# Kernel optimization log

Hardware: AMD Instinct MI355X
Metric: run time of the kernel (lower is better)

Reference implementation:

```python
import jax, jax.numpy as jnp
import numpy as np

B, S, P, D, H = 2, 2048, 2048, 2048, 16
HD = D // H  # head_dim = 128


def setup_inputs() -> dict:
    key = jax.random.key(0)
    ks = jax.random.split(key, 8)
    scale = 1.0 / np.sqrt(D)
    return {
        "x": jax.random.normal(ks[0], (B, S, D), jnp.float32),
        "cache_k": jax.random.normal(ks[1], (B, P, D), jnp.float32),
        "cache_v": jax.random.normal(ks[2], (B, P, D), jnp.float32),
        "wq": jax.random.normal(ks[3], (D, D), jnp.float32) * scale,
        "bq": jnp.zeros((D,), jnp.float32),
        "wk": jax.random.normal(ks[4], (D, D), jnp.float32) * scale,
        "bk": jnp.zeros((D,), jnp.float32),
        "wv": jax.random.normal(ks[5], (D, D), jnp.float32) * scale,
        "bv": jnp.zeros((D,), jnp.float32),
        "wo": jax.random.normal(ks[6], (D, D), jnp.float32) * scale,
        "bo": jnp.zeros((D,), jnp.float32),
    }


def reference(x, cache_k, cache_v, wq, bq, wk, bk, wv, bv, wo, bo):
    bsz, seq_len, _ = x.shape
    q = x @ wq + bq                      # [B,S,D]
    k_new = x @ wk + bk                  # [B,S,D]
    v_new = x @ wv + bv
    # use_cache=True path: prepend cached (detached) keys/values
    k = jnp.concatenate([cache_k, k_new], axis=1)  # [B,P+S,D]
    v = jnp.concatenate([cache_v, v_new], axis=1)
    # split heads: [B,H,S,hd] / [B,H,K,hd]
    q = q.reshape(bsz, seq_len, H, HD).transpose(0, 2, 1, 3)
    k = k.reshape(bsz, -1, H, HD).transpose(0, 2, 1, 3)
    v = v.reshape(bsz, -1, H, HD).transpose(0, 2, 1, 3)
    scores = jnp.einsum("bhsd,bhkd->bhsk", q, k) / jnp.sqrt(jnp.float32(HD))
    attn = jax.nn.softmax(scores, axis=-1)          # full-softmax, no mask
    out = jnp.einsum("bhsk,bhkd->bhsd", attn, v)
    out = out.transpose(0, 2, 1, 3).reshape(bsz, seq_len, D)
    return out @ wo + bo
```

## Files before the change

kernel.cpp:

```cpp
#include <hip/hip_runtime.h>

typedef __attribute__((ext_vector_type(8))) short short8;
typedef __attribute__((ext_vector_type(4))) short short4_;
typedef __attribute__((ext_vector_type(4))) float f32x4;

#define AS1 __attribute__((address_space(1)))
#define AS3 __attribute__((address_space(3)))
#define GLD16(g, l) __builtin_amdgcn_global_load_lds((const AS1 void*)(g), (AS3 void*)(l), 16, 0, 0)

#define C2 0.12751743f

__device__ __forceinline__ unsigned short f2bf(float f) {
  unsigned int u = __float_as_uint(f);
  u += 0x7fffu + ((u >> 16) & 1u);
  return (unsigned short)(u >> 16);
}

__global__ __launch_bounds__(256) void k_transpose_w(
    const float* __restrict__ wq, const float* __restrict__ wk,
    const float* __restrict__ wv, const float* __restrict__ wo,
    unsigned short* __restrict__ wqkvT, unsigned short* __restrict__ woT)
{
  __shared__ float tile[64][65];
  const int z = blockIdx.z;
  const float* src = (z == 0) ? wq : (z == 1) ? wk : (z == 2) ? wv : wo;
  unsigned short* dst = (z == 3) ? woT : (wqkvT + (size_t)z * 2048 * 2048);
  const int k0 = blockIdx.y * 64, n0 = blockIdx.x * 64;
  const int tid = threadIdx.x;
#pragma unroll
  for (int p = 0; p < 4; ++p) {
    const int r = p * 16 + (tid >> 4);
    const int c = (tid & 15) * 4;
    f32x4 v = *(const f32x4*)(src + (size_t)(k0 + r) * 2048 + n0 + c);
    tile[r][c + 0] = v[0]; tile[r][c + 1] = v[1];
    tile[r][c + 2] = v[2]; tile[r][c + 3] = v[3];
  }
  __syncthreads();
#pragma unroll
  for (int p = 0; p < 2; ++p) {
    const int task = tid + p * 256;
    const int n = task >> 3;
    const int kc = (task & 7) * 8;
    short8 ov;
#pragma unroll
    for (int j = 0; j < 8; ++j) ov[j] = (short)f2bf(tile[kc + j][n]);
    *(short8*)(dst + (size_t)(n0 + n) * 2048 + k0 + kc) = ov;
  }
}

__global__ __launch_bounds__(256) void k_convert(
    const float* __restrict__ x, const float* __restrict__ ck, const float* __restrict__ cv,
    unsigned short* __restrict__ xbf, unsigned short* __restrict__ kfull,
    unsigned short* __restrict__ vfull)
{
  const int z = blockIdx.y;
  const size_t idx = ((size_t)blockIdx.x * 256 + threadIdx.x) * 8;
  const float* src = (z == 0) ? x : (z == 1) ? ck : cv;
  f32x4 a = *(const f32x4*)(src + idx);
  f32x4 b = *(const f32x4*)(src + idx + 4);
  short8 ov;
#pragma unroll
  for (int j = 0; j < 4; ++j) { ov[j] = (short)f2bf(a[j]); ov[j + 4] = (short)f2bf(b[j]); }
  unsigned short* dp; size_t di;
  if (z == 0) { dp = xbf; di = idx; }
  else {
    const size_t r = idx >> 11, cl = idx & 2047;
    const size_t orow = r + (r & ~(size_t)2047);
    di = orow * 2048 + cl;
    dp = (z == 1) ? kfull : vfull;
  }
  *(short8*)(dp + di) = ov;
}

template <int MODE>
__global__ __launch_bounds__(256, 2) void k_gemm(
    const unsigned short* __restrict__ A, const unsigned short* __restrict__ BT,
    unsigned short* __restrict__ Oq, unsigned short* __restrict__ Ok,
    unsigned short* __restrict__ Ov, float* __restrict__ Of,
    const float* __restrict__ b0, const float* __restrict__ b1,
    const float* __restrict__ b2, int K)
{
  __shared__ unsigned short Ah[128 * 32];
  __shared__ unsigned short Bh[128 * 32];
  const int tid = threadIdx.x;
  const int l = tid & 63, w = tid >> 6;
  const int l15 = l & 15, g = l >> 4;
  const int wr = (w >> 1) * 64, wc = (w & 1) * 64;
  const int bm = blockIdx.y, bn = blockIdx.x;
  const unsigned short* Ab = A + (size_t)bm * 128 * K;
  const unsigned short* Bb = BT + (size_t)bn * 128 * K;
  const int srow = l >> 2;
  const int scol = (l & 3) * 8;
  f32x4 acc[4][4];
#pragma unroll
  for (int i = 0; i < 4; ++i)
#pragma unroll
    for (int j = 0; j < 4; ++j)
#pragma unroll
      for (int e = 0; e < 4; ++e) acc[i][j][e] = 0.f;

  for (int kt = 0; kt < K; kt += 32) {
#pragma unroll
    for (int cc = 0; cc < 2; ++cc) {
      const int c = w + cc * 4;
      GLD16(Ab + (size_t)(c * 16 + srow) * K + kt + scol, &Ah[c * 512]);
      GLD16(Bb + (size_t)(c * 16 + srow) * K + kt + scol, &Bh[c * 512]);
    }
    __syncthreads();
    short8 af[4], bf[4];
#pragma unroll
    for (int i = 0; i < 4; ++i) {
      af[i] = *(const short8*)&Ah[(wr + i * 16 + l15) * 32 + g * 8];
      bf[i] = *(const short8*)&Bh[(wc + i * 16 + l15) * 32 + g * 8];
    }
#pragma unroll
    for (int i = 0; i < 4; ++i)
#pragma unroll
      for (int j = 0; j < 4; ++j)
        acc[i][j] = __builtin_amdgcn_mfma_f32_16x16x32_bf16(af[i], bf[j], acc[i][j], 0, 0, 0);
    __syncthreads();
  }

  const int rbase = bm * 128 + wr + g * 4;
  if (MODE == 0) {
    const int nglob = bn * 128;
    const int which = nglob >> 11;
    const int ncol0 = nglob & 2047;
    unsigned short* dst = (which == 0) ? Oq : (which == 1) ? Ok : Ov;
    const float* bias = (which == 0) ? b0 : (which == 1) ? b1 : b2;
#pragma unroll
    for (int j = 0; j < 4; ++j) {
      const int cc = ncol0 + wc + j * 16 + l15;
      const float bb = bias[cc];
#pragma unroll
      for (int i = 0; i < 4; ++i) {
#pragma unroll
        for (int ii = 0; ii < 4; ++ii) {
          const int rr = rbase + i * 16 + ii;
          const size_t orow = (which == 0) ? (size_t)rr
                                           : (size_t)(rr + (rr & ~2047) + 2048);
          dst[orow * 2048 + cc] = f2bf(acc[i][j][ii] + bb);
        }
      }
    }
  } else {
#pragma unroll
    for (int j = 0; j < 4; ++j) {
      const int cc = bn * 128 + wc + j * 16 + l15;
      const float bb = b0[cc];
#pragma unroll
      for (int i = 0; i < 4; ++i) {
#pragma unroll
        for (int ii = 0; ii < 4; ++ii) {
          const int rr = rbase + i * 16 + ii;
          Of[(size_t)rr * 2048 + cc] = acc[i][j][ii] + bb;
        }
      }
    }
  }
}

__global__ __launch_bounds__(256, 2) void k_flash(
    const unsigned short* __restrict__ qbuf, const unsigned short* __restrict__ kfull,
    const unsigned short* __restrict__ vfull, unsigned short* __restrict__ attnout)
{
  __shared__ char smem[65536];
  unsigned short* Kl = (unsigned short*)smem;
  unsigned short* Vt = (unsigned short*)(smem + 32768);
  const int tid = threadIdx.x;
  const int l = tid & 63, w = tid >> 6;
  const int l15 = l & 15, g = l >> 4, l7 = l & 7;
  const int qt = blockIdx.x, bh = blockIdx.y;
  const int b = bh >> 4, h = bh & 15;

  short8 qf[4];
  {
    const int qrow = qt * 64 + w * 16 + l15;
    const unsigned short* qp = qbuf + ((size_t)(b * 2048 + qrow)) * 2048 + h * 128 + g * 8;
    qf[0] = *(const short8*)(qp);
    qf[1] = *(const short8*)(qp + 32);
    qf[2] = *(const short8*)(qp + 64);
    qf[3] = *(const short8*)(qp + 96);
  }
  f32x4 o[8];
#pragma unroll
  for (int d = 0; d < 8; ++d)
#pragma unroll
    for (int e = 0; e < 4; ++e) o[d][e] = 0.f;
  float m = -3.0e38f, lsum = 0.f;

  const int srowK = l >> 4;
  const int suK = l & 15;

  for (int t = 0; t < 32; ++t) {
    const size_t kt0 = (size_t)t * 128;
    const unsigned short* kb = kfull + ((size_t)b * 4096 + kt0) * 2048 + h * 128;
    const unsigned short* vb = vfull + ((size_t)b * 4096 + kt0) * 2048 + h * 128;
#pragma unroll
    for (int ci = 0; ci < 8; ++ci) {
      const int c = w * 8 + ci;
      const int row = c * 4 + srowK;
      const int ucol = (suK ^ (row & 7)) * 8;
      GLD16(kb + (size_t)row * 2048 + ucol, &Kl[c * 512]);
    }
#pragma unroll
    for (int p = 0; p < 2; ++p) {
      const int task = tid + p * 256;
      const int g4 = task & 31;
      const int dc = task >> 5;
      const unsigned short* vp = vb + (size_t)(g4 * 4) * 2048 + dc * 8;
      short8 r0 = *(const short8*)(vp);
      short8 r1 = *(const short8*)(vp + 2048);
      short8 r2 = *(const short8*)(vp + 4096);
      short8 r3 = *(const short8*)(vp + 6144);
      const int vcol4 = (g4 & ~7) | ((g4 & 3) << 1) | ((g4 >> 2) & 1);
#pragma unroll
      for (int d = 0; d < 8; ++d) {
        const int row = dc * 8 + d;
        short4_ pk; pk[0] = r0[d]; pk[1] = r1[d]; pk[2] = r2[d]; pk[3] = r3[d];
        const int unit16 = (vcol4 >> 1) ^ (row & 7);
        *(short4_*)((char*)Vt + row * 256 + unit16 * 16 + (vcol4 & 1) * 8) = pk;
      }
    }
    __syncthreads();
    f32x4 sc[8];
#pragma unroll
    for (int kc = 0; kc < 8; ++kc) {
      f32x4 a4;
#pragma unroll
      for (int e = 0; e < 4; ++e) a4[e] = 0.f;
      const int row = kc * 16 + l15;
#pragma unroll
      for (int kk = 0; kk < 4; ++kk) {
        const int unit = (kk * 4 + g) ^ (row & 7);
        short8 af = *(const short8*)((const char*)Kl + row * 256 + unit * 16);
        a4 = __builtin_amdgcn_mfma_f32_16x16x32_bf16(af, qf[kk], a4, 0, 0, 0);
      }
      sc[kc] = a4;
    }
    float tm = -3.0e38f;
#pragma unroll
    for (int kc = 0; kc < 8; ++kc)
#pragma unroll
      for (int i = 0; i < 4; ++i) tm = fmaxf(tm, sc[kc][i]);
    tm = fmaxf(tm, __shfl_xor(tm, 16, 64));
    tm = fmaxf(tm, __shfl_xor(tm, 32, 64));
    const float mnew = fmaxf(m, tm);
    const float f = exp2f(C2 * (m - mnew));
    m = mnew;
    float psum = 0.f;
    short8 pf[4];
#pragma unroll
    for (int c = 0; c < 4; ++c) {
#pragma unroll
      for (int i = 0; i < 4; ++i) {
        const float p0 = exp2f(C2 * (sc[2 * c][i] - mnew));
        const float p1 = exp2f(C2 * (sc[2 * c + 1][i] - mnew));
        psum += p0 + p1;
        pf[c][i] = (short)f2bf(p0);
        pf[c][i + 4] = (short)f2bf(p1);
      }
    }
    psum += __shfl_xor(psum, 16, 64);
    psum += __shfl_xor(psum, 32, 64);
    lsum = lsum * f + psum;
#pragma unroll
    for (int d = 0; d < 8; ++d)
#pragma unroll
      for (int e = 0; e < 4; ++e) o[d][e] *= f;
#pragma unroll
    for (int c = 0; c < 4; ++c) {
#pragma unroll
      for (int d = 0; d < 8; ++d) {
        const int row = d * 16 + l15;
        const int unit = (4 * c + g) ^ l7;
        short8 vf = *(const short8*)((const char*)Vt + row * 256 + unit * 16);
        o[d] = __builtin_amdgcn_mfma_f32_16x16x32_bf16(vf, pf[c], o[d], 0, 0, 0);
      }
    }
    __syncthreads();
  }
  const float inv = 1.0f / lsum;
  float* ep = (float*)smem;
#pragma unroll
  for (int d = 0; d < 8; ++d) {
    f32x4 tv;
#pragma unroll
    for (int e = 0; e < 4; ++e) tv[e] = o[d][e] * inv;
    *(f32x4*)(ep + (w * 16 + l15) * 132 + d * 16 + g * 4) = tv;
  }
  __syncthreads();
#pragma unroll
  for (int p = 0; p < 4; ++p) {
    const int task = tid + p * 256;
    const int row = task >> 4, ch = task & 15;
    const float* sp = ep + row * 132 + ch * 8;
    short8 ov;
#pragma unroll
    for (int j = 0; j < 8; ++j) ov[j] = (short)f2bf(sp[j]);
    const int qg = qt * 64 + row;
    *(short8*)(attnout + ((size_t)(b * 2048 + qg)) * 2048 + h * 128 + ch * 8) = ov;
  }
}

extern "C" void kernel_launch(void* const* d_in, const int* in_sizes, int n_in,
                              void* d_out, int out_size, void* d_ws, size_t ws_size,
                              hipStream_t stream)
{
  const float* x  = (const float*)d_in[0];
  const float* ck = (const float*)d_in[1];
  const float* cv = (const float*)d_in[2];
  const float* wq = (const float*)d_in[3];
  const float* bq = (const float*)d_in[4];
  const float* wk = (const float*)d_in[5];
  const float* bk = (const float*)d_in[6];
  const float* wv = (const float*)d_in[7];
  const float* bv = (const float*)d_in[8];
  const float* wo = (const float*)d_in[9];
  const float* bo = (const float*)d_in[10];
  float* out = (float*)d_out;

  char* ws = (char*)d_ws;
  unsigned short* xbf   = (unsigned short*)(ws);
  unsigned short* wqkvT = (unsigned short*)(ws + 16777216ull);
  unsigned short* woT   = (unsigned short*)(ws + 41943040ull);
  unsigned short* qbuf  = (unsigned short*)(ws + 50331648ull);
  unsigned short* kfull = (unsigned short*)(ws + 67108864ull);
  unsigned short* vfull = (unsigned short*)(ws + 100663296ull);
  unsigned short* aout  = (unsigned short*)(ws + 134217728ull);

  k_transpose_w<<<dim3(32, 32, 4), 256, 0, stream>>>(wq, wk, wv, wo, wqkvT, woT);
  k_convert<<<dim3(4096, 3), 256, 0, stream>>>(x, ck, cv, xbf, kfull, vfull);
  k_gemm<0><<<dim3(48, 32), 256, 0, stream>>>(xbf, wqkvT, qbuf, kfull, vfull, nullptr,
                                              bq, bk, bv, 2048);
  k_flash<<<dim3(32, 32), 256, 0, stream>>>(qbuf, kfull, vfull, aout);
  k_gemm<1><<<dim3(16, 32), 256, 0, stream>>>(aout, woT, nullptr, nullptr, nullptr, out,
                                              bo, nullptr, nullptr, 2048);
}
```

Before: 682.8 us.

## Double-buffer K/V tiles, process two query tiles per wave, lazy rescale

Rewrites the flash-attention kernel so each block handles 128 query rows (two 16-row sets per wave) and reuses every K/V fragment loaded from LDS for both sets. K/V tiles shrink to 64 keys and are double-buffered, so the next tile is prefetched while the current one is computed, and priority hints are added around the MFMA sections. The running-max rescale is skipped unless the max grows by more than a threshold, and the epilogue now goes through bf16 staging. Risks are higher register pressure with two accumulator sets, and half as many blocks in the grid.

```diff
diff --git a/kernel.cpp b/kernel.cpp
--- a/kernel.cpp
+++ b/kernel.cpp
@@ -165,141 +165,212 @@
     const unsigned short* __restrict__ vfull, unsigned short* __restrict__ attnout)
 {
   __shared__ char smem[65536];
-  unsigned short* Kl = (unsigned short*)smem;
-  unsigned short* Vt = (unsigned short*)(smem + 32768);
   const int tid = threadIdx.x;
   const int l = tid & 63, w = tid >> 6;
-  const int l15 = l & 15, g = l >> 4, l7 = l & 7;
+  const int l15 = l & 15, g = l >> 4;
   const int qt = blockIdx.x, bh = blockIdx.y;
   const int b = bh >> 4, h = bh & 15;
 
-  short8 qf[4];
+  short8 qfA[4], qfB[4];
   {
-    const int qrow = qt * 64 + w * 16 + l15;
-    const unsigned short* qp = qbuf + ((size_t)(b * 2048 + qrow)) * 2048 + h * 128 + g * 8;
-    qf[0] = *(const short8*)(qp);
-    qf[1] = *(const short8*)(qp + 32);
-    qf[2] = *(const short8*)(qp + 64);
-    qf[3] = *(const short8*)(qp + 96);
-  }
-  f32x4 o[8];
+    const int qrowA = qt * 128 + w * 32 + l15;
+    const unsigned short* qpA = qbuf + ((size_t)(b * 2048 + qrowA)) * 2048 + h * 128 + g * 8;
+    const unsigned short* qpB = qpA + 16 * 2048;
+#pragma unroll
+    for (int kk = 0; kk < 4; ++kk) {
+      qfA[kk] = *(const short8*)(qpA + kk * 32);
+      qfB[kk] = *(const short8*)(qpB + kk * 32);
+    }
+  }
+  f32x4 oA[8], oB[8];
 #pragma unroll
   for (int d = 0; d < 8; ++d)
 #pragma unroll
-    for (int e = 0; e < 4; ++e) o[d][e] = 0.f;
-  float m = -3.0e38f, lsum = 0.f;
-
-  const int srowK = l >> 4;
-  const int suK = l & 15;
-
-  for (int t = 0; t < 32; ++t) {
-    const size_t kt0 = (size_t)t * 128;
-    const unsigned short* kb = kfull + ((size_t)b * 4096 + kt0) * 2048 + h * 128;
-    const unsigned short* vb = vfull + ((size_t)b * 4096 + kt0) * 2048 + h * 128;
-#pragma unroll
-    for (int ci = 0; ci < 8; ++ci) {
-      const int c = w * 8 + ci;
-      const int row = c * 4 + srowK;
-      const int ucol = (suK ^ (row & 7)) * 8;
-      GLD16(kb + (size_t)row * 2048 + ucol, &Kl[c * 512]);
-    }
-#pragma unroll
-    for (int p = 0; p < 2; ++p) {
-      const int task = tid + p * 256;
-      const int g4 = task & 31;
-      const int dc = task >> 5;
-      const unsigned short* vp = vb + (size_t)(g4 * 4) * 2048 + dc * 8;
-      short8 r0 = *(const short8*)(vp);
-      short8 r1 = *(const short8*)(vp + 2048);
-      short8 r2 = *(const short8*)(vp + 4096);
-      short8 r3 = *(const short8*)(vp + 6144);
-      const int vcol4 = (g4 & ~7) | ((g4 & 3) << 1) | ((g4 >> 2) & 1);
+    for (int e = 0; e < 4; ++e) { oA[d][e] = 0.f; oB[d][e] = 0.f; }
+  float mA = -1e30f, mB = -1e30f, lsA = 0.f, lsB = 0.f;
+
+  const unsigned short* kbase = kfull + ((size_t)b * 4096) * 2048 + h * 128;
+  const unsigned short* vbase = vfull + ((size_t)b * 4096) * 2048 + h * 128;
+
+  const int vg4 = tid & 15;
+  const int vdc = tid >> 4;
+  const int vcol4 = (vg4 & 8) | ((vg4 & 3) << 1) | ((vg4 >> 2) & 1);
+  const int vu = vcol4 >> 1;
+  const int vhalf = (vcol4 & 1) * 8;
+  const int ksrow = l >> 4, ksu = l & 15;
+
+  auto STAGEK = [&](int t, char* Kn) {
+    const unsigned short* kb = kbase + (size_t)t * 64 * 2048;
+#pragma unroll
+    for (int ci = 0; ci < 4; ++ci) {
+      const int c = w * 4 + ci;
+      const int row = c * 4 + ksrow;
+      GLD16(kb + (size_t)row * 2048 + ((ksu ^ (row & 7)) * 8), Kn + c * 1024);
+    }
+  };
+  auto VLOAD = [&](int t, short8* r) {
+    const unsigned short* vp = vbase + ((size_t)t * 64 + vg4 * 4) * 2048 + vdc * 8;
+    r[0] = *(const short8*)(vp);
+    r[1] = *(const short8*)(vp + 2048);
+    r[2] = *(const short8*)(vp + 4096);
+    r[3] = *(const short8*)(vp + 6144);
+  };
+  auto VWRITE = [&](char* Vn, short8* r) {
+#pragma unroll
+    for (int d = 0; d < 8; ++d) {
+      const int row = vdc * 8 + d;
+      const int mm = (d ^ vdc) & 7;
+      short4_ pk; pk[0] = r[0][d]; pk[1] = r[1][d]; pk[2] = r[2][d]; pk[3] = r[3][d];
+      *(short4_*)(Vn + row * 128 + ((vu ^ mm) * 16) + vhalf) = pk;
+    }
+  };
+
+  {
+    short8 vr[4];
+    STAGEK(0, smem);
+    VLOAD(0, vr);
+    VWRITE(smem + 16384, vr);
+    __syncthreads();
+  }
+
+  for (int t = 0; t < 64; ++t) {
+    char* Kc = smem + (t & 1) * 32768;
+    char* Vc = Kc + 16384;
+    char* Kn = smem + ((t + 1) & 1) * 32768;
+    char* Vn = Kn + 16384;
+    const bool pre = (t + 1) < 64;
+    short8 vr[4];
+    if (pre) {
+      STAGEK(t + 1, Kn);
+      VLOAD(t + 1, vr);
+    }
+    f32x4 scA[4], scB[4];
+    __builtin_amdgcn_s_setprio(1);
+#pragma unroll
+    for (int kc = 0; kc < 4; ++kc) {
+      f32x4 a0, a1;
+#pragma unroll
+      for (int e = 0; e < 4; ++e) { a0[e] = 0.f; a1[e] = 0.f; }
+      const int rowk = kc * 16 + l15;
+      const int mk = rowk & 7;
+#pragma unroll
+      for (int kk = 0; kk < 4; ++kk) {
+        short8 kf = *(const short8*)(Kc + rowk * 256 + (((kk * 4 + g) ^ mk) * 16));
+        a0 = __builtin_amdgcn_mfma_f32_16x16x32_bf16(kf, qfA[kk], a0, 0, 0, 0);
+        a1 = __builtin_amdgcn_mfma_f32_16x16x32_bf16(kf, qfB[kk], a1, 0, 0, 0);
+      }
+      scA[kc] = a0; scB[kc] = a1;
+    }
+    __builtin_amdgcn_s_setprio(0);
+    if (pre) VWRITE(Vn, vr);
+
+    short8 pfA[2], pfB[2];
+    {
+      float tm = fmaxf(fmaxf(scA[0][0], scA[0][1]), fmaxf(scA[0][2], scA[0][3]));
+#pragma unroll
+      for (int kc = 1; kc < 4; ++kc)
+        tm = fmaxf(tm, fmaxf(fmaxf(scA[kc][0], scA[kc][1]), fmaxf(scA[kc][2], scA[kc][3])));
+      tm = fmaxf(tm, __shfl_xor(tm, 16, 64));
+      tm = fmaxf(tm, __shfl_xor(tm, 32, 64));
+      if (!__all(tm <= mA + 16.f)) {
+        const float mn = fmaxf(mA, tm);
+        const float f = exp2f(C2 * (mA - mn));
+        mA = mn; lsA *= f;
+#pragma unroll
+        for (int d = 0; d < 8; ++d)
+#pragma unroll
+          for (int e = 0; e < 4; ++e) oA[d][e] *= f;
+      }
+      const float mc = C2 * mA;
+      float ps = 0.f;
+#pragma unroll
+      for (int c = 0; c < 2; ++c) {
+#pragma unroll
+        for (int i = 0; i < 4; ++i) {
+          const float p0 = exp2f(fmaf(C2, scA[2 * c][i], -mc));
+          const float p1 = exp2f(fmaf(C2, scA[2 * c + 1][i], -mc));
+          ps += p0 + p1;
+          pfA[c][i] = (short)f2bf(p0);
+          pfA[c][i + 4] = (short)f2bf(p1);
+        }
+      }
+      ps += __shfl_xor(ps, 16, 64);
+      ps += __shfl_xor(ps, 32, 64);
+      lsA += ps;
+    }
+    {
+      float tm = fmaxf(fmaxf(scB[0][0], scB[0][1]), fmaxf(scB[0][2], scB[0][3]));
+#pragma unroll
+      for (int kc = 1; kc < 4; ++kc)
+        tm = fmaxf(tm, fmaxf(fmaxf(scB[kc][0], scB[kc][1]), fmaxf(scB[kc][2], scB[kc][3])));
+      tm = fmaxf(tm, __shfl_xor(tm, 16, 64));
+      tm = fmaxf(tm, __shfl_xor(tm, 32, 64));
+      if (!__all(tm <= mB + 16.f)) {
+        const float mn = fmaxf(mB, tm);
+        const float f = exp2f(C2 * (mB - mn));
+        mB = mn; lsB *= f;
+#pragma unroll
+        for (int d = 0; d < 8; ++d)
+#pragma unroll
+          for (int e = 0; e < 4; ++e) oB[d][e] *= f;
+      }
+      const float mc = C2 * mB;
+      float ps = 0.f;
+#pragma unroll
+      for (int c = 0; c < 2; ++c) {
+#pragma unroll
+        for (int i = 0; i < 4; ++i) {
+          const float p0 = exp2f(fmaf(C2, scB[2 * c][i], -mc));
+          const float p1 = exp2f(fmaf(C2, scB[2 * c + 1][i], -mc));
+          ps += p0 + p1;
+          pfB[c][i] = (short)f2bf(p0);
+          pfB[c][i + 4] = (short)f2bf(p1);
+        }
+      }
+      ps += __shfl_xor(ps, 16, 64);
+      ps += __shfl_xor(ps, 32, 64);
+      lsB += ps;
+    }
+
+    __builtin_amdgcn_s_setprio(1);
+#pragma unroll
+    for (int c = 0; c < 2; ++c) {
 #pragma unroll
       for (int d = 0; d < 8; ++d) {
-        const int row = dc * 8 + d;
-        short4_ pk; pk[0] = r0[d]; pk[1] = r1[d]; pk[2] = r2[d]; pk[3] = r3[d];
-        const int unit16 = (vcol4 >> 1) ^ (row & 7);
-        *(short4_*)((char*)Vt + row * 256 + unit16 * 16 + (vcol4 & 1) * 8) = pk;
-      }
-    }
+        const int rowv = d * 16 + l15;
+        const int mv = (rowv ^ (rowv >> 3)) & 7;
+        short8 vf = *(const short8*)(Vc + rowv * 128 + ((((c * 4 + g) ^ mv)) * 16));
+        oA[d] = __builtin_amdgcn_mfma_f32_16x16x32_bf16(vf, pfA[c], oA[d], 0, 0, 0);
+        oB[d] = __builtin_amdgcn_mfma_f32_16x16x32_bf16(vf, pfB[c], oB[d], 0, 0, 0);
+      }
+    }
+    __builtin_amdgcn_s_setprio(0);
     __syncthreads();
-    f32x4 sc[8];
-#pragma unroll
-    for (int kc = 0; kc < 8; ++kc) {
-      f32x4 a4;
-#pragma unroll
-      for (int e = 0; e < 4; ++e) a4[e] = 0.f;
-      const int row = kc * 16 + l15;
-#pragma unroll
-      for (int kk = 0; kk < 4; ++kk) {
-        const int unit = (kk * 4 + g) ^ (row & 7);
-        short8 af = *(const short8*)((const char*)Kl + row * 256 + unit * 16);
-        a4 = __builtin_amdgcn_mfma_f32_16x16x32_bf16(af, qf[kk], a4, 0, 0, 0);
-      }
-      sc[kc] = a4;
-    }
-    float tm = -3.0e38f;
-#pragma unroll
-    for (int kc = 0; kc < 8; ++kc)
-#pragma unroll
-      for (int i = 0; i < 4; ++i) tm = fmaxf(tm, sc[kc][i]);
-    tm = fmaxf(tm, __shfl_xor(tm, 16, 64));
-    tm = fmaxf(tm, __shfl_xor(tm, 32, 64));
-    const float mnew = fmaxf(m, tm);
-    const float f = exp2f(C2 * (m - mnew));
-    m = mnew;
-    float psum = 0.f;
-    short8 pf[4];
-#pragma unroll
-    for (int c = 0; c < 4; ++c) {
-#pragma unroll
-      for (int i = 0; i < 4; ++i) {
-        const float p0 = exp2f(C2 * (sc[2 * c][i] - mnew));
-        const float p1 = exp2f(C2 * (sc[2 * c + 1][i] - mnew));
-        psum += p0 + p1;
-        pf[c][i] = (short)f2bf(p0);
-        pf[c][i + 4] = (short)f2bf(p1);
-      }
-    }
-    psum += __shfl_xor(psum, 16, 64);
-    psum += __shfl_xor(psum, 32, 64);
-    lsum = lsum * f + psum;
-#pragma unroll
-    for (int d = 0; d < 8; ++d)
-#pragma unroll
-      for (int e = 0; e < 4; ++e) o[d][e] *= f;
-#pragma unroll
-    for (int c = 0; c < 4; ++c) {
-#pragma unroll
-      for (int d = 0; d < 8; ++d) {
-        const int row = d * 16 + l15;
-        const int unit = (4 * c + g) ^ l7;
-        short8 vf = *(const short8*)((const char*)Vt + row * 256 + unit * 16);
-        o[d] = __builtin_amdgcn_mfma_f32_16x16x32_bf16(vf, pf[c], o[d], 0, 0, 0);
-      }
-    }
-    __syncthreads();
-  }
-  const float inv = 1.0f / lsum;
-  float* ep = (float*)smem;
+  }
+
+  __syncthreads();
+  const float invA = 1.0f / lsA, invB = 1.0f / lsB;
+  char* ep = smem;
 #pragma unroll
   for (int d = 0; d < 8; ++d) {
-    f32x4 tv;
-#pragma unroll
-    for (int e = 0; e < 4; ++e) tv[e] = o[d][e] * inv;
-    *(f32x4*)(ep + (w * 16 + l15) * 132 + d * 16 + g * 4) = tv;
+    short4_ pa, pb;
+#pragma unroll
+    for (int e = 0; e < 4; ++e) {
+      pa[e] = (short)f2bf(oA[d][e] * invA);
+      pb[e] = (short)f2bf(oB[d][e] * invB);
+    }
+    const int colb = (d * 16 + g * 4) * 2;
+    *(short4_*)(ep + (w * 32 + l15) * 272 + colb) = pa;
+    *(short4_*)(ep + (w * 32 + 16 + l15) * 272 + colb) = pb;
   }
   __syncthreads();
 #pragma unroll
-  for (int p = 0; p < 4; ++p) {
-    const int task = tid + p * 256;
-    const int row = task >> 4, ch = task & 15;
-    const float* sp = ep + row * 132 + ch * 8;
-    short8 ov;
-#pragma unroll
-    for (int j = 0; j < 8; ++j) ov[j] = (short)f2bf(sp[j]);
-    const int qg = qt * 64 + row;
-    *(short8*)(attnout + ((size_t)(b * 2048 + qg)) * 2048 + h * 128 + ch * 8) = ov;
+  for (int i = 0; i < 8; ++i) {
+    const int task = tid + i * 256;
+    const int row = task >> 4, un = task & 15;
+    short8 ov = *(const short8*)(ep + row * 272 + un * 16);
+    const int qg = qt * 128 + row;
+    *(short8*)(attnout + ((size_t)(b * 2048 + qg)) * 2048 + h * 128 + un * 8) = ov;
   }
 }
 
@@ -333,7 +404,7 @@
   k_convert<<<dim3(4096, 3), 256, 0, stream>>>(x, ck, cv, xbf, kfull, vfull);
   k_gemm<0><<<dim3(48, 32), 256, 0, stream>>>(xbf, wqkvT, qbuf, kfull, vfull, nullptr,
                                               bq, bk, bv, 2048);
-  k_flash<<<dim3(32, 32), 256, 0, stream>>>(qbuf, kfull, vfull, aout);
+  k_flash<<<dim3(16, 32), 256, 0, stream>>>(qbuf, kfull, vfull, aout);
   k_gemm<1><<<dim3(16, 32), 256, 0, stream>>>(aout, woT, nullptr, nullptr, nullptr, out,
                                               bo, nullptr, nullptr, 2048);
 }
```

Measured after the change: 555.7 us. 18.6% less time.
